# Optimization experiments

Measured on AMD Instinct MI355X. Metric: run time of the kernel, lower is better.

## Reference

```python
import jax, jax.numpy as jnp
import numpy as np

B, L, M, H = 4096, 512, 17, 17  # batch, seq_len, num_features, latent_dim


def setup_inputs() -> dict:
    key = jax.random.key(0)
    ks = jax.random.split(key, 5)
    s = 1.0 / np.sqrt(H)  # torch nn.LSTM init scale
    x = jax.random.normal(ks[0], (B, L, M), dtype=jnp.float32)
    W_ih = jax.random.uniform(ks[1], (4 * H, M), dtype=jnp.float32, minval=-s, maxval=s)
    W_hh = jax.random.uniform(ks[2], (4 * H, H), dtype=jnp.float32, minval=-s, maxval=s)
    b_ih = jax.random.uniform(ks[3], (4 * H,), dtype=jnp.float32, minval=-s, maxval=s)
    b_hh = jax.random.uniform(ks[4], (4 * H,), dtype=jnp.float32, minval=-s, maxval=s)
    return {"x": x, "W_ih": W_ih, "W_hh": W_hh, "b_ih": b_ih, "b_hh": b_hh}


def _lstm(x, W_ih, W_hh, b_ih, b_hh):
    # Precompute input projections for all timesteps in one GEMM: (B,L,4H)
    xW = jnp.einsum('blm,gm->blg', x, W_ih) + b_ih + b_hh
    xW_t = jnp.swapaxes(xW, 0, 1)  # (L,B,4H) for scan over time
    W_hh_T = W_hh.T  # (H,4H)

    def step(carry, xw_t):
        h, c = carry
        gates = xw_t + h @ W_hh_T  # (B,4H)
        i, f, g, o = jnp.split(gates, 4, axis=-1)  # torch gate order: i,f,g,o
        i = jax.nn.sigmoid(i)
        f = jax.nn.sigmoid(f)
        g = jnp.tanh(g)
        o = jax.nn.sigmoid(o)
        c_new = f * c + i * g
        h_new = o * jnp.tanh(c_new)
        return (h_new, c_new), h_new

    h0 = jnp.zeros((x.shape[0], W_hh.shape[1]), dtype=x.dtype)
    c0 = jnp.zeros_like(h0)
    (h_f, c_f), hs = jax.lax.scan(step, (h0, c0), xW_t)
    out = jnp.swapaxes(hs, 0, 1)  # (B,L,H)
    return out, h_f, c_f


def reference(x, W_ih, W_hh, b_ih, b_hh):
    out, h_f, c_f = _lstm(x, W_ih, W_hh, b_ih, b_hh)
    # match torch return: out, (h,c) with leading num_layers dim, and x
    return out, (h_f[None], c_f[None]), x
```

## Files before the change

kernel.cpp:

```cpp
#include <hip/hip_runtime.h>
#include <hip/hip_bf16.h>


namespace {
constexpr int B_TOT = 4096;
constexpr int L_SEQ = 512;
constexpr int NF    = 17;
constexpr int BS    = 16;
constexpr int TPB   = 320;
constexpr int TC    = 32;
constexpr int NCHUNK = L_SEQ / TC;
constexpr int KPAD  = 24;
constexpr int F4_PER_ROW   = TC * NF / 4;
constexpr int F4_PER_CHUNK = BS * F4_PER_ROW;
constexpr int PF_MAX = (F4_PER_CHUNK + TPB - 1) / TPB;

constexpr int OUT_H = B_TOT * L_SEQ * NF;
constexpr int OUT_C = OUT_H + B_TOT * NF;
constexpr int OUT_X = OUT_C + B_TOT * NF;
}

typedef __attribute__((ext_vector_type(8))) short bf16x8;
typedef __attribute__((ext_vector_type(4))) float f32x4;

__device__ __forceinline__ unsigned short f2bf(float f) {
  union { float f; unsigned int u; } v; v.f = f;
  unsigned int r = v.u + 0x7fff + ((v.u >> 16) & 1);
  return (unsigned short)(r >> 16);
}
__device__ __forceinline__ float sigm(float x) {
  return __builtin_amdgcn_rcpf(1.f + __expf(-x));
}
__device__ __forceinline__ float tanh_fast(float x) {
  float e = __expf(2.f * x);
  return 1.f - 2.f * __builtin_amdgcn_rcpf(e + 1.f);
}

__device__ __forceinline__ void block_sync_lds() {
  asm volatile("s_waitcnt lgkmcnt(0)" ::: "memory");
  __builtin_amdgcn_s_barrier();
  asm volatile("" ::: "memory");
}

__global__ void __launch_bounds__(TPB) lstm_kernel(
    const float* __restrict__ x, const float* __restrict__ W_ih,
    const float* __restrict__ W_hh, const float* __restrict__ b_ih,
    const float* __restrict__ b_hh, float* __restrict__ out)
{
  __shared__ __align__(16) unsigned short x_s[2][TC][BS][KPAD];
  __shared__ __align__(16) unsigned short h_s[2][BS][KPAD];
  __shared__ __align__(16) unsigned short w0_s[80][32];
  __shared__ __align__(16) unsigned short w1_s[80][32];
  __shared__ __align__(16) float bias_s[80];
  __shared__ __align__(16) unsigned short zero16[8];

  const int tid  = threadIdx.x;
  const int lane = tid & 63;
  const int T    = tid >> 6;
  const int bb   = lane & 15;
  const int q    = lane >> 4;
  const int b0   = blockIdx.x * BS;

  f32x4 pf[PF_MAX];
  #pragma unroll
  for (int i = 0; i < PF_MAX; ++i) {
    int u = tid + TPB * i;
    if (u < F4_PER_CHUNK) {
      int row = u / F4_PER_ROW, off = u % F4_PER_ROW;
      pf[i] = *(const f32x4*)(x + ((b0 + row) * L_SEQ) * NF + off * 4);
    }
  }

  {
    unsigned int* p = (unsigned int*)&x_s[0][0][0][0];
    for (int u = tid; u < (int)(sizeof(x_s) / 4); u += TPB) p[u] = 0;
    unsigned int* ph = (unsigned int*)&h_s[0][0][0];
    for (int u = tid; u < (int)(sizeof(h_s) / 4); u += TPB) ph[u] = 0;
    if (tid < 4) ((unsigned int*)zero16)[tid] = 0;
  }
  for (int u = tid; u < 80 * 32; u += TPB) {
    int r = u >> 5, k = u & 31;
    unsigned short v0 = 0, v1 = 0;
    int j = -1, ty = 0;
    if (r < 64)      { j = r >> 2; ty = r & 3; }
    else if (r < 68) { j = 16;     ty = r - 64; }
    if (j >= 0 && k < NF) {
      int g = ty * NF + j;
      v0 = f2bf(W_ih[g * NF + k]);
      v1 = f2bf(W_hh[g * NF + k]);
    }
    w0_s[r][k] = v0; w1_s[r][k] = v1;
  }
  for (int u = tid; u < 80; u += TPB) {
    float bv = 0.f; int j = -1, ty = 0;
    if (u < 64)      { j = u >> 2; ty = u & 3; }
    else if (u < 68) { j = 16;     ty = u - 64; }
    if (j >= 0) { int g = ty * NF + j; bv = b_ih[g] + b_hh[g]; }
    bias_s[u] = bv;
  }
  __syncthreads();

  auto stage = [&](int cn) {
    #pragma unroll
    for (int i = 0; i < PF_MAX; ++i) {
      int u = tid + TPB * i;
      if (u < F4_PER_CHUNK) {
        int row = u / F4_PER_ROW, off = u % F4_PER_ROW;
        int gidx = ((b0 + row) * L_SEQ + cn * TC) * NF + off * 4;
        *(f32x4*)(out + OUT_X + gidx) = pf[i];
        int p = off * 4, tl = p / NF, m = p - tl * NF;
        #pragma unroll
        for (int e = 0; e < 4; ++e) {
          x_s[cn & 1][tl][row][m] = f2bf(pf[i][e]);
          if (++m == NF) { m = 0; ++tl; }
        }
      }
    }
  };
  auto prefetch = [&](int cn) {
    #pragma unroll
    for (int i = 0; i < PF_MAX; ++i) {
      int u = tid + TPB * i;
      if (u < F4_PER_CHUNK) {
        int row = u / F4_PER_ROW, off = u % F4_PER_ROW;
        pf[i] = *(const f32x4*)(x + ((b0 + row) * L_SEQ + cn * TC) * NF + off * 4);
      }
    }
  };

  stage(0);
  prefetch(1);

  const bf16x8 a0 = *(const bf16x8*)&w0_s[16 * T + bb][q * 8];
  const bf16x8 a1 = *(const bf16x8*)&w1_s[16 * T + bb][q * 8];
  const f32x4 bias4 = *(const f32x4*)&bias_s[16 * T + q * 4];

  const int j = 4 * T + q;
  const bool active = (T < 4) || (q == 0);
  const int jj = (j > 16) ? 16 : j;

  const unsigned short* xbuf[2] = {
    (q == 3) ? zero16 : &x_s[0][0][bb][q * 8],
    (q == 3) ? zero16 : &x_s[1][0][bb][q * 8] };
  const int xstep = (q == 3) ? 0 : BS * KPAD;
  const unsigned short* hr[2] = {
    (q == 3) ? zero16 : &h_s[0][bb][q * 8],
    (q == 3) ? zero16 : &h_s[1][bb][q * 8] };
  unsigned short* hw[2] = { &h_s[1][bb][jj], &h_s[0][bb][jj] };

  float c_st = 0.f, h_last = 0.f;
  float* outp = out + (b0 + bb) * L_SEQ * NF + jj;

  for (int c = 0; c < NCHUNK; ++c) {
    const unsigned short* xp = xbuf[c & 1];
    for (int tt = 0; tt < TC; ++tt) {
      const int t = c * TC + tt;
      block_sync_lds();
      bf16x8 bx = *(const bf16x8*)xp;
      bf16x8 bh = *(const bf16x8*)hr[t & 1];
      xp += xstep;
      f32x4 acc = __builtin_amdgcn_mfma_f32_16x16x32_bf16(a0, bx, bias4, 0, 0, 0);
      acc       = __builtin_amdgcn_mfma_f32_16x16x32_bf16(a1, bh, acc,   0, 0, 0);
      if (active) {
        float gi = sigm(acc[0]);
        float gf = sigm(acc[1]);
        float gg = tanh_fast(acc[2]);
        float go = sigm(acc[3]);
        c_st  = gf * c_st + gi * gg;
        h_last = go * tanh_fast(c_st);
        *hw[t & 1] = f2bf(h_last);
        outp[0] = h_last;
        outp += NF;
      }
    }
    if (c + 1 < NCHUNK) {
      stage(c + 1);
      if (c + 2 < NCHUNK) prefetch(c + 2);
    }
  }

  if (active) {
    out[OUT_H + (b0 + bb) * NF + j] = h_last;
    out[OUT_C + (b0 + bb) * NF + j] = c_st;
  }
}

extern "C" void kernel_launch(void* const* d_in, const int* in_sizes, int n_in,
                              void* d_out, int out_size, void* d_ws, size_t ws_size,
                              hipStream_t stream) {
  (void)in_sizes; (void)n_in; (void)out_size; (void)d_ws; (void)ws_size;
  const float* x    = (const float*)d_in[0];
  const float* W_ih = (const float*)d_in[1];
  const float* W_hh = (const float*)d_in[2];
  const float* b_ih = (const float*)d_in[3];
  const float* b_hh = (const float*)d_in[4];
  float* out = (float*)d_out;
  hipLaunchKernelGGL(lstm_kernel, dim3(B_TOT / BS), dim3(TPB), 0, stream,
                     x, W_ih, W_hh, b_ih, b_hh, out);
}
```

Baseline: 499.2 us.

## Software-pipeline input-projection MFMA off the recurrent critical path, unroll time loop

Computes the next timestep's input-projection MFMA (x·W_ih + bias) during the current step, so each serial step only waits on the recurrent h·W_hh MFMA. The time loop is unrolled by two with fixed even/odd h buffer pointers, which removes the indexed pointer arrays. The bf16 conversion of h now uses the hardware v_cvt_pk_bf16_f32 instruction in place of the manual rounding sequence. The extra accumulators raise register pressure, and the inline asm depends on that instruction being available on this target.

```diff
diff --git a/kernel.cpp b/kernel.cpp
--- a/kernel.cpp
+++ b/kernel.cpp
@@ -27,6 +27,11 @@
   union { float f; unsigned int u; } v; v.f = f;
   unsigned int r = v.u + 0x7fff + ((v.u >> 16) & 1);
   return (unsigned short)(r >> 16);
+}
+__device__ __forceinline__ unsigned short h2bf(float f) {
+  unsigned int r;
+  asm("v_cvt_pk_bf16_f32 %0, %1, %2" : "=v"(r) : "v"(f), "v"(f));
+  return (unsigned short)r;
 }
 __device__ __forceinline__ float sigm(float x) {
   return __builtin_amdgcn_rcpf(1.f + __expf(-x));
@@ -139,39 +144,60 @@
   const bool active = (T < 4) || (q == 0);
   const int jj = (j > 16) ? 16 : j;
 
-  const unsigned short* xbuf[2] = {
-    (q == 3) ? zero16 : &x_s[0][0][bb][q * 8],
-    (q == 3) ? zero16 : &x_s[1][0][bb][q * 8] };
+  const unsigned short* const xbase0 = (q == 3) ? zero16 : &x_s[0][0][bb][q * 8];
+  const unsigned short* const xbase1 = (q == 3) ? zero16 : &x_s[1][0][bb][q * 8];
   const int xstep = (q == 3) ? 0 : BS * KPAD;
-  const unsigned short* hr[2] = {
-    (q == 3) ? zero16 : &h_s[0][bb][q * 8],
-    (q == 3) ? zero16 : &h_s[1][bb][q * 8] };
-  unsigned short* hw[2] = { &h_s[1][bb][jj], &h_s[0][bb][jj] };
+  const unsigned short* const hr0 = (q == 3) ? zero16 : &h_s[0][bb][q * 8];
+  const unsigned short* const hr1 = (q == 3) ? zero16 : &h_s[1][bb][q * 8];
+  unsigned short* const hw0 = &h_s[1][bb][jj];
+  unsigned short* const hw1 = &h_s[0][bb][jj];
 
   float c_st = 0.f, h_last = 0.f;
   float* outp = out + (b0 + bb) * L_SEQ * NF + jj;
 
+  auto epilogue = [&](const f32x4& acc, unsigned short* hwp) {
+    if (active) {
+      float gi = sigm(acc[0]);
+      float gf = sigm(acc[1]);
+      float gg = tanh_fast(acc[2]);
+      float go = sigm(acc[3]);
+      c_st   = gf * c_st + gi * gg;
+      h_last = go * tanh_fast(c_st);
+      *hwp = h2bf(h_last);
+      outp[0] = h_last;
+      outp += NF;
+    }
+  };
+
+  f32x4 accx_e{}, accx_o{};
+
   for (int c = 0; c < NCHUNK; ++c) {
-    const unsigned short* xp = xbuf[c & 1];
-    for (int tt = 0; tt < TC; ++tt) {
-      const int t = c * TC + tt;
+    const unsigned short* xp = (c & 1) ? xbase1 : xbase0;
+    #pragma unroll
+    for (int tt = 0; tt < TC; tt += 2) {
       block_sync_lds();
-      bf16x8 bx = *(const bf16x8*)xp;
-      bf16x8 bh = *(const bf16x8*)hr[t & 1];
-      xp += xstep;
-      f32x4 acc = __builtin_amdgcn_mfma_f32_16x16x32_bf16(a0, bx, bias4, 0, 0, 0);
-      acc       = __builtin_amdgcn_mfma_f32_16x16x32_bf16(a1, bh, acc,   0, 0, 0);
-      if (active) {
-        float gi = sigm(acc[0]);
-        float gf = sigm(acc[1]);
-        float gg = tanh_fast(acc[2]);
-        float go = sigm(acc[3]);
-        c_st  = gf * c_st + gi * gg;
-        h_last = go * tanh_fast(c_st);
-        *hw[t & 1] = f2bf(h_last);
-        outp[0] = h_last;
-        outp += NF;
-      }
+      if (tt == 0) {
+        bf16x8 bx = *(const bf16x8*)xp;
+        accx_e = __builtin_amdgcn_mfma_f32_16x16x32_bf16(a0, bx, bias4, 0, 0, 0);
+      }
+      {
+        bf16x8 bh = *(const bf16x8*)hr0;
+        f32x4 acc = __builtin_amdgcn_mfma_f32_16x16x32_bf16(a1, bh, accx_e, 0, 0, 0);
+        bf16x8 bxo = *(const bf16x8*)(xp + xstep);
+        accx_o = __builtin_amdgcn_mfma_f32_16x16x32_bf16(a0, bxo, bias4, 0, 0, 0);
+        epilogue(acc, hw0);
+      }
+      block_sync_lds();
+      {
+        bf16x8 bh = *(const bf16x8*)hr1;
+        f32x4 acc = __builtin_amdgcn_mfma_f32_16x16x32_bf16(a1, bh, accx_o, 0, 0, 0);
+        if (tt + 2 < TC) {
+          bf16x8 bxe = *(const bf16x8*)(xp + 2 * xstep);
+          accx_e = __builtin_amdgcn_mfma_f32_16x16x32_bf16(a0, bxe, bias4, 0, 0, 0);
+        }
+        epilogue(acc, hw1);
+      }
+      xp += 2 * xstep;
     }
     if (c + 1 < NCHUNK) {
       stage(c + 1);
```

New measurement: 465.9 us. 6.7% less time.
